# Optimization experiments

Hardware: AMD Instinct MI355X
Metric: run time of the kernel (lower is better)

Reference implementation:

```python
import jax, jax.numpy as jnp
import numpy as np

N_CELLS = 1024
HID = 256
IN_DIM = 256
OUT_DIM = 256
NOISE_DIM = 32
N_LOOP = 32  # min(32, n_cells)


def _lin(x, W, b):
    # torch nn.Linear: y = x @ W.T + b, W shape [out, in]
    return x @ W.T + b


def faction_sync_debate(h, step, n_factions=8, sync=0.15, debate=0.15):
    n, d = h.shape
    n_f = min(n_factions, n // 2)
    if n_f < 2:
        return h
    fs = n // n_f  # assumes n_f * fs == n (true for 1024/8)
    blk = h.reshape(n_f, fs, d)
    # per-faction mean pull (disjoint slices -> order independent)
    blk = (1.0 - sync) * blk + sync * blk.mean(axis=1, keepdims=True)
    if step > 5:  # step is a Python int -> static branch
        global_opinion = blk.mean(axis=1).mean(axis=0)  # [d]
        dc = max(1, fs // 4)
        blk = blk.at[:, :dc, :].set((1.0 - debate) * blk[:, :dc, :] + debate * global_opinion)
    return blk.reshape(n, d)


def setup_inputs() -> dict:
    key = jax.random.key(0)
    ks = iter(jax.random.split(key, 32))

    def rn(shape, scale=0.02):
        return (jax.random.normal(next(ks), shape, dtype=jnp.float32) * scale)

    flat = N_CELLS * HID  # 262144
    inp = {
        "x": rn((1, IN_DIM), 1.0),
        "noise": rn((1, NOISE_DIM), 1.0),
        "cell_hiddens": rn((N_CELLS, HID), 0.1),
        # generator: Linear(in+32,256) -> ReLU -> Linear(256,512) -> ReLU -> Linear(512, flat)
        "gen_W1": rn((256, IN_DIM + NOISE_DIM)), "gen_b1": rn((256,)),
        "gen_W2": rn((512, 256)), "gen_b2": rn((512,)),
        "gen_W3": rn((flat, 512)), "gen_b3": rn((flat,)),
        # discriminator: Linear(flat,512) -> LReLU(0.2) -> Linear(512,256) -> LReLU -> Linear(256,1) -> Sigmoid
        "disc_W1": rn((512, flat)), "disc_b1": rn((512,)),
        "disc_W2": rn((256, 512)), "disc_b2": rn((256,)),
        "disc_W3": rn((1, 256)), "disc_b3": rn((1,)),
        # mind engines: Linear(in+hid,128) -> ReLU -> Linear(128,out)
        "ea_W1": rn((128, IN_DIM + HID)), "ea_b1": rn((128,)),
        "ea_W2": rn((OUT_DIM, 128)), "ea_b2": rn((OUT_DIM,)),
        "eg_W1": rn((128, IN_DIM + HID)), "eg_b1": rn((128,)),
        "eg_W2": rn((OUT_DIM, 128)), "eg_b2": rn((OUT_DIM,)),
        # GRUCell(out+1, hid): gate order r, z, n
        "gru_Wih": rn((3 * HID, OUT_DIM + 1)), "gru_bih": rn((3 * HID,)),
        "gru_Whh": rn((3 * HID, HID)), "gru_bhh": rn((3 * HID,)),
        "step": 10,
    }
    return inp


def reference(x, noise, cell_hiddens,
              gen_W1, gen_b1, gen_W2, gen_b2, gen_W3, gen_b3,
              disc_W1, disc_b1, disc_W2, disc_b2, disc_W3, disc_b3,
              ea_W1, ea_b1, ea_W2, ea_b2, eg_W1, eg_b1, eg_W2, eg_b2,
              gru_Wih, gru_bih, gru_Whh, gru_bhh, step):
    sg = jax.lax.stop_gradient
    # --- generate_states ---
    gi = jnp.concatenate([x, noise], axis=-1)           # [1, in+32]
    h1 = jax.nn.relu(_lin(gi, gen_W1, gen_b1))
    h2 = jax.nn.relu(_lin(h1, gen_W2, gen_b2))
    gen_states = _lin(h2, gen_W3, gen_b3).reshape(N_CELLS, HID)
    # torch: gen_states.detach() then faction sync+debate
    synced = faction_sync_debate(sg(gen_states), step)
    # --- batched BenchMind over first 32 cells (replaces Python loop) ---
    H = synced[:N_LOOP]                                  # [32, HID]
    X = jnp.broadcast_to(x, (N_LOOP, x.shape[-1]))       # [32, IN]
    comb = jnp.concatenate([X, H], axis=-1)              # [32, IN+HID]
    a = _lin(jax.nn.relu(_lin(comb, ea_W1, ea_b1)), ea_W2, ea_b2)
    g = _lin(jax.nn.relu(_lin(comb, eg_W1, eg_b1)), eg_W2, eg_b2)
    outputs = a - g                                      # [32, OUT]
    tensions = (outputs ** 2).mean(axis=-1)              # [32]
    # GRUCell update (mem inputs detached as in torch)
    mem_in = jnp.concatenate([sg(outputs), sg(tensions)[:, None]], axis=-1)  # [32, OUT+1]
    gih = _lin(mem_in, gru_Wih, gru_bih)
    ghh = _lin(H, gru_Whh, gru_bhh)
    ir, iz, i_n = jnp.split(gih, 3, axis=-1)
    hr, hz, h_n = jnp.split(ghh, 3, axis=-1)
    r = jax.nn.sigmoid(ir + hr)
    z = jax.nn.sigmoid(iz + hz)
    n_cand = jnp.tanh(i_n + r * h_n)
    new_hiddens = (1.0 - z) * n_cand + z * H             # [32, HID]
    # --- buffer update (no_grad) + discriminate ---
    new_cell_hiddens = sg(0.7 * synced + 0.3 * cell_hiddens)

    def disc(s):
        f = s.reshape(1, -1)
        d1 = jax.nn.leaky_relu(_lin(f, disc_W1, disc_b1), 0.2)
        d2 = jax.nn.leaky_relu(_lin(d1, disc_W2, disc_b2), 0.2)
        return jax.nn.sigmoid(_lin(d2, disc_W3, disc_b3))

    d_real = disc(new_cell_hiddens)
    d_fake = disc(gen_states)
    # tensions were .item()'d in torch -> constants
    mean_tension = sg(tensions).mean()
    w = jax.nn.softmax(sg(tensions))                     # [32]
    combined = (w[:, None] * outputs).sum(axis=0, keepdims=True)  # [1, OUT]
    return combined, mean_tension, d_real, d_fake, new_hiddens
```

## Files before the change

### kernel.cpp

```cpp
#include <hip/hip_runtime.h>
#include <math.h>

#define N_CELLS 1024
#define HID     256
#define IN_DIM  256
#define NOISE_DIM 32
#define OUT_DIM 256
#define N_LOOP  32
#define FLAT    (N_CELLS*HID)

__device__ __forceinline__ float wave_reduce64(float v) {
    #pragma unroll
    for (int m = 32; m; m >>= 1) v += __shfl_xor(v, m);
    return v;
}

__global__ void k_gen_h1(const float* __restrict__ x, const float* __restrict__ noise,
                         const float* __restrict__ W1, const float* __restrict__ b1,
                         float* __restrict__ h1) {
    __shared__ __align__(16) float gi[288];
    int t = threadIdx.x, l = t & 63, w = t >> 6;
    gi[t] = x[t];
    if (t < 32) gi[256 + t] = noise[t];
    __syncthreads();
    int j = blockIdx.x * 4 + w;
    const float4* wr = (const float4*)(W1 + j * 288);
    const float4* g4 = (const float4*)gi;
    float4 a = wr[l], v = g4[l];
    float acc = a.x*v.x + a.y*v.y + a.z*v.z + a.w*v.w;
    if (l < 8) {
        float4 a2 = wr[64 + l], v2 = g4[64 + l];
        acc += a2.x*v2.x + a2.y*v2.y + a2.z*v2.z + a2.w*v2.w;
    }
    acc = wave_reduce64(acc);
    if (l == 0) h1[j] = fmaxf(acc + b1[j], 0.f);
}

__global__ void k_gen_h2(const float* __restrict__ h1, const float* __restrict__ W2,
                         const float* __restrict__ b2, float* __restrict__ h2) {
    int t = threadIdx.x, l = t & 63, w = t >> 6;
    int j = blockIdx.x * 4 + w;
    float4 a = ((const float4*)(W2 + j * 256))[l];
    float4 v = ((const float4*)h1)[l];
    float acc = a.x*v.x + a.y*v.y + a.z*v.z + a.w*v.w;
    acc = wave_reduce64(acc);
    if (l == 0) h2[j] = fmaxf(acc + b2[j], 0.f);
}

__global__ void k_gen_big(const float* __restrict__ W3, const float* __restrict__ b3,
                          const float* __restrict__ h2, float* __restrict__ gs) {
    int lane = threadIdx.x & 63;
    int row  = blockIdx.x * (blockDim.x >> 6) + (threadIdx.x >> 6);
    const float4* h24 = (const float4*)h2;
    float4 ha = h24[lane], hb = h24[64 + lane];
    const float4* w4 = (const float4*)(W3 + (size_t)row * 512);
    float4 wa = w4[lane], wb = w4[64 + lane];
    float acc = wa.x*ha.x + wa.y*ha.y + wa.z*ha.z + wa.w*ha.w
              + wb.x*hb.x + wb.y*hb.y + wb.z*hb.z + wb.w*hb.w;
    acc = wave_reduce64(acc);
    if (lane == 0) gs[row] = acc + b3[row];
}

__global__ void k_fmean(const float* __restrict__ gs, float* __restrict__ fmean) {
    __shared__ float part[4][64];
    int b = blockIdx.x, t = threadIdx.x;
    int f = b >> 2, q = b & 3;
    int c = q * 64 + (t & 63), rg = t >> 6;
    const float* base = gs + (size_t)(f * 128 + rg * 32) * 256 + c;
    float s = 0.f;
    for (int i = 0; i < 32; ++i) s += base[(size_t)i * 256];
    part[rg][t & 63] = s;
    __syncthreads();
    if (t < 64) {
        float v = part[0][t] + part[1][t] + part[2][t] + part[3][t];
        fmean[f * 256 + q * 64 + t] = v * (1.f / 128.f);
    }
}

__global__ void k_sync(const float* __restrict__ gs, const float* __restrict__ fmean,
                       const float* __restrict__ ch, const int* __restrict__ step,
                       float* __restrict__ Hbuf, float* __restrict__ ncn) {
    int c = blockIdx.x, d = threadIdx.x;
    int f = c >> 7;
    float gm = 0.f;
    #pragma unroll
    for (int k = 0; k < 8; ++k) gm += fmean[k * 256 + d];
    gm *= 0.125f;
    float fm = fmean[f * 256 + d];
    float v = 0.85f * gs[c * 256 + d] + 0.15f * fm;
    if (((c & 127) < 32) && (*step > 5)) v = 0.85f * v + 0.15f * gm;
    ncn[c * 256 + d] = 0.7f * v + 0.3f * ch[c * 256 + d];
    if (c < N_LOOP) Hbuf[c * 256 + d] = v;
}

__global__ void k_mega(const float* __restrict__ dW1, const float* __restrict__ db1,
                       const float* __restrict__ ncn, const float* __restrict__ gs,
                       const float* __restrict__ x, const float* __restrict__ Hbuf,
                       const float* __restrict__ eaW1, const float* __restrict__ eab1,
                       const float* __restrict__ eaW2, const float* __restrict__ eab2,
                       const float* __restrict__ egW1, const float* __restrict__ egb1,
                       const float* __restrict__ egW2, const float* __restrict__ egb2,
                       const float* __restrict__ Wih, const float* __restrict__ bih,
                       const float* __restrict__ Whh, const float* __restrict__ bhh,
                       float* __restrict__ d1r, float* __restrict__ d1f,
                       float* __restrict__ outputs, float* __restrict__ tensions,
                       float* __restrict__ out) {
    __shared__ float sR[16];
    __shared__ float sF[16];
    __shared__ __align__(16) float xh[512];
    __shared__ __align__(16) float hag[256];
    __shared__ __align__(16) float outs[256];
    __shared__ float red[256];
    __shared__ float rzA[512];
    __shared__ float inb[256];
    __shared__ float hnb[256];
    __shared__ float tsh;
    int b = blockIdx.x, t = threadIdx.x, l = t & 63, w = t >> 6;

    if (b >= 32) {
        int row = b - 32;
        const float4* w4 = (const float4*)(dW1 + (size_t)row * FLAT);
        const float4* r4 = (const float4*)ncn;
        const float4* f4 = (const float4*)gs;
        float aR = 0.f, aF = 0.f;
        for (int i = t; i < FLAT / 4; i += 1024) {
            float4 ww = w4[i], r = r4[i], f = f4[i];
            aR += ww.x*r.x + ww.y*r.y + ww.z*r.z + ww.w*r.w;
            aF += ww.x*f.x + ww.y*f.y + ww.z*f.z + ww.w*f.w;
        }
        aR = wave_reduce64(aR);
        aF = wave_reduce64(aF);
        if (l == 0) { sR[w] = aR; sF[w] = aF; }
        __syncthreads();
        if (t < 16) {
            float r = sR[t], f = sF[t];
            #pragma unroll
            for (int m = 8; m; m >>= 1) { r += __shfl_xor(r, m); f += __shfl_xor(f, m); }
            if (t == 0) { d1r[row] = r + db1[row]; d1f[row] = f + db1[row]; }
        }
        return;
    }

    int i = b;
    if (t < 512) xh[t] = (t < 256) ? x[t] : Hbuf[i * 256 + (t - 256)];
    __syncthreads();

    for (int k = 0; k < 16; ++k) {
        int j = w * 16 + k;
        const float* W = (j < 128) ? (eaW1 + (size_t)j * 512) : (egW1 + (size_t)(j - 128) * 512);
        const float4* w4 = (const float4*)W;
        const float4* v4 = (const float4*)xh;
        float4 a = w4[l], v = v4[l];
        float acc = a.x*v.x + a.y*v.y + a.z*v.z + a.w*v.w;
        float4 a2 = w4[64 + l], v2 = v4[64 + l];
        acc += a2.x*v2.x + a2.y*v2.y + a2.z*v2.z + a2.w*v2.w;
        acc = wave_reduce64(acc);
        if (l == 0) {
            float bias = (j < 128) ? eab1[j] : egb1[j - 128];
            hag[j] = fmaxf(acc + bias, 0.f);
        }
    }
    __syncthreads();

    for (int k = 0; k < 16; ++k) {
        int tr = w * 16 + k;
        int sl = l & 31;
        bool lo = (l < 32);
        const float4* wv4 = lo ? (const float4*)(eaW2 + (size_t)tr * 128)
                               : (const float4*)(egW2 + (size_t)tr * 128);
        const float4* h4 = (const float4*)(hag + (lo ? 0 : 128));
        float4 a = wv4[sl], v = h4[sl];
        float d_ = a.x*v.x + a.y*v.y + a.z*v.z + a.w*v.w;
        float acc = lo ? d_ : -d_;
        acc = wave_reduce64(acc);
        if (l == 0) {
            float o = acc + eab2[tr] - egb2[tr];
            outs[tr] = o;
            outputs[i * 256 + tr] = o;
        }
    }
    __syncthreads();

    if (t < 256) red[t] = outs[t] * outs[t];
    __syncthreads();
    for (int m = 128; m; m >>= 1) { if (t < m && t + m < 256) red[t] += red[t + m]; __syncthreads(); }
    if (t == 0) { float tn = red[0] * (1.f / 256.f); tensions[i] = tn; tsh = tn; }
    __syncthreads();
    float tn = tsh;

    {
        float4 ov = ((const float4*)outs)[l];
        float4 Hv = ((const float4*)(xh + 256))[l];
        for (int k = 0; k < 48; ++k) {
            int u = w * 48 + k;
            const float* wr = Wih + (size_t)u * 257;
            float g0 = wr[4*l]*ov.x + wr[4*l+1]*ov.y + wr[4*l+2]*ov.z + wr[4*l+3]*ov.w;
            if (l == 0) g0 += wr[256] * tn;
            float4 wh = ((const float4*)(Whh + (size_t)u * 256))[l];
            float h0 = wh.x*Hv.x + wh.y*Hv.y + wh.z*Hv.z + wh.w*Hv.w;
            if (u < 512) {
                float s = wave_reduce64(g0 + h0);
                if (l == 0) rzA[u] = s + bih[u] + bhh[u];
            } else {
                float sg = wave_reduce64(g0);
                float sh = wave_reduce64(h0);
                if (l == 0) { inb[u - 512] = sg + bih[u]; hnb[u - 512] = sh + bhh[u]; }
            }
        }
    }
    __syncthreads();

    if (t < 256) {
        float r = 1.f / (1.f + expf(-rzA[t]));
        float z = 1.f / (1.f + expf(-rzA[256 + t]));
        float nc = tanhf(inb[t] + r * hnb[t]);
        float Hd = xh[256 + t];
        out[259 + i * 256 + t] = (1.f - z) * nc + z * Hd;
    }
}

__global__ void k_epi(const float* __restrict__ W2, const float* __restrict__ b2,
                      const float* __restrict__ W3, const float* __restrict__ b3,
                      const float* __restrict__ d1r, const float* __restrict__ d1f,
                      const float* __restrict__ outputs, const float* __restrict__ tensions,
                      float* __restrict__ out) {
    int b = blockIdx.x, t = threadIdx.x;
    if (b < 2) {
        __shared__ __align__(16) float lv[512];
        __shared__ float l2[256];
        __shared__ float red[256];
        const float* d1 = b ? d1f : d1r;
        for (int j = t; j < 512; j += 256) { float v = d1[j]; lv[j] = v > 0.f ? v : 0.2f * v; }
        __syncthreads();
        {
            float acc = b2[t];
            const float4* wr = (const float4*)(W2 + t * 512);
            const float4* l4 = (const float4*)lv;
            for (int k = 0; k < 128; ++k) {
                float4 w = wr[k], v = l4[k];
                acc += w.x*v.x + w.y*v.y + w.z*v.z + w.w*v.w;
            }
            l2[t] = acc > 0.f ? acc : 0.2f * acc;
        }
        __syncthreads();
        red[t] = l2[t] * W3[t];
        __syncthreads();
        for (int m = 128; m; m >>= 1) { if (t < m) red[t] += red[t + m]; __syncthreads(); }
        if (t == 0) { float v = red[0] + b3[0]; out[257 + b] = 1.f / (1.f + expf(-v)); }
    } else {
        __shared__ float w[32];
        __shared__ float ts[32];
        if (t < 32) ts[t] = tensions[t];
        __syncthreads();
        if (t == 0) {
            float mx = ts[0];
            for (int i = 1; i < 32; ++i) mx = fmaxf(mx, ts[i]);
            float s = 0.f, mean = 0.f;
            for (int i = 0; i < 32; ++i) { float e = expf(ts[i] - mx); w[i] = e; s += e; mean += ts[i]; }
            float inv = 1.f / s;
            for (int i = 0; i < 32; ++i) w[i] *= inv;
            out[256] = mean * (1.f / 32.f);
        }
        __syncthreads();
        float c = 0.f;
        for (int i = 0; i < 32; ++i) c += w[i] * outputs[i * 256 + t];
        out[t] = c;
    }
}

extern "C" void kernel_launch(void* const* d_in, const int* in_sizes, int n_in,
                              void* d_out, int out_size, void* d_ws, size_t ws_size,
                              hipStream_t stream) {
    const float* x     = (const float*)d_in[0];
    const float* noise = (const float*)d_in[1];
    const float* ch    = (const float*)d_in[2];
    const float* gW1   = (const float*)d_in[3];
    const float* gb1   = (const float*)d_in[4];
    const float* gW2   = (const float*)d_in[5];
    const float* gb2   = (const float*)d_in[6];
    const float* gW3   = (const float*)d_in[7];
    const float* gb3   = (const float*)d_in[8];
    const float* dW1   = (const float*)d_in[9];
    const float* db1   = (const float*)d_in[10];
    const float* dW2   = (const float*)d_in[11];
    const float* db2   = (const float*)d_in[12];
    const float* dW3   = (const float*)d_in[13];
    const float* db3   = (const float*)d_in[14];
    const float* eaW1  = (const float*)d_in[15];
    const float* eab1  = (const float*)d_in[16];
    const float* eaW2  = (const float*)d_in[17];
    const float* eab2  = (const float*)d_in[18];
    const float* egW1  = (const float*)d_in[19];
    const float* egb1  = (const float*)d_in[20];
    const float* egW2  = (const float*)d_in[21];
    const float* egb2  = (const float*)d_in[22];
    const float* Wih   = (const float*)d_in[23];
    const float* bih   = (const float*)d_in[24];
    const float* Whh   = (const float*)d_in[25];
    const float* bhh   = (const float*)d_in[26];
    const int*   step  = (const int*)d_in[27];

    float* out = (float*)d_out;
    float* ws  = (float*)d_ws;
    float* h1buf    = ws;
    float* h2       = h1buf + 256;
    float* gs       = h2 + 512;
    float* ncn      = gs + 262144;
    float* fmean    = ncn + 262144;
    float* Hbuf     = fmean + 2048;
    float* outputs  = Hbuf + 8192;
    float* tensions = outputs + 8192;
    float* d1r      = tensions + 32;
    float* d1f      = d1r + 512;

    k_gen_h1<<<64, 256, 0, stream>>>(x, noise, gW1, gb1, h1buf);
    k_gen_h2<<<128, 256, 0, stream>>>(h1buf, gW2, gb2, h2);
    k_gen_big<<<FLAT / 4, 256, 0, stream>>>(gW3, gb3, h2, gs);
    k_fmean<<<32, 256, 0, stream>>>(gs, fmean);
    k_sync<<<1024, 256, 0, stream>>>(gs, fmean, ch, step, Hbuf, ncn);
    k_mega<<<544, 1024, 0, stream>>>(dW1, db1, ncn, gs, x, Hbuf,
                                     eaW1, eab1, eaW2, eab2,
                                     egW1, egb1, egW2, egb2,
                                     Wih, bih, Whh, bhh,
                                     d1r, d1f, outputs, tensions, out);
    k_epi<<<3, 256, 0, stream>>>(dW2, db2, dW3, db3, d1r, d1f, outputs, tensions, out);
}
```

Measured before the change: 292.6 us.

## Fuse faction sync into discriminator kernel, batch gen rows, split epilogue

The separate sync kernel that wrote the 1 MB ncn and Hbuf buffers is removed. The discriminator blocks now recompute the synced and new cell hiddens on the fly from gs, ch and the faction means held in shared memory, and the engine blocks rebuild their H row directly. The big generator GEMV now computes four rows per wave and writes them with a vectorized store. The fmean loop is unrolled into four accumulators, and the epilogue is split into an 8-block layer-2 GEMV plus a 1-block tail. This saves one launch and a large write/read round trip, at the cost of extra ALU work and one more epilogue launch.

Result: no change. 295.8 us (+1.1%).

```diff
diff --git a/kernel.cpp b/kernel.cpp
--- a/kernel.cpp
+++ b/kernel.cpp
@@ -14,6 +14,9 @@
     for (int m = 32; m; m >>= 1) v += __shfl_xor(v, m);
     return v;
 }
+__device__ __forceinline__ float dot4(float4 a, float4 b) {
+    return a.x*b.x + a.y*b.y + a.z*b.z + a.w*b.w;
+}
 
 __global__ void k_gen_h1(const float* __restrict__ x, const float* __restrict__ noise,
                          const float* __restrict__ W1, const float* __restrict__ b1,
@@ -27,10 +30,10 @@
     const float4* wr = (const float4*)(W1 + j * 288);
     const float4* g4 = (const float4*)gi;
     float4 a = wr[l], v = g4[l];
-    float acc = a.x*v.x + a.y*v.y + a.z*v.z + a.w*v.w;
+    float acc = dot4(a, v);
     if (l < 8) {
         float4 a2 = wr[64 + l], v2 = g4[64 + l];
-        acc += a2.x*v2.x + a2.y*v2.y + a2.z*v2.z + a2.w*v2.w;
+        acc += dot4(a2, v2);
     }
     acc = wave_reduce64(acc);
     if (l == 0) h1[j] = fmaxf(acc + b1[j], 0.f);
@@ -42,23 +45,41 @@
     int j = blockIdx.x * 4 + w;
     float4 a = ((const float4*)(W2 + j * 256))[l];
     float4 v = ((const float4*)h1)[l];
-    float acc = a.x*v.x + a.y*v.y + a.z*v.z + a.w*v.w;
+    float acc = dot4(a, v);
     acc = wave_reduce64(acc);
     if (l == 0) h2[j] = fmaxf(acc + b2[j], 0.f);
 }
 
 __global__ void k_gen_big(const float* __restrict__ W3, const float* __restrict__ b3,
                           const float* __restrict__ h2, float* __restrict__ gs) {
-    int lane = threadIdx.x & 63;
-    int row  = blockIdx.x * (blockDim.x >> 6) + (threadIdx.x >> 6);
+    int t = threadIdx.x, l = t & 63, w = t >> 6;
+    int r0 = blockIdx.x * 16 + w * 4;
     const float4* h24 = (const float4*)h2;
-    float4 ha = h24[lane], hb = h24[64 + lane];
-    const float4* w4 = (const float4*)(W3 + (size_t)row * 512);
-    float4 wa = w4[lane], wb = w4[64 + lane];
-    float acc = wa.x*ha.x + wa.y*ha.y + wa.z*ha.z + wa.w*ha.w
-              + wb.x*hb.x + wb.y*hb.y + wb.z*hb.z + wb.w*hb.w;
-    acc = wave_reduce64(acc);
-    if (lane == 0) gs[row] = acc + b3[row];
+    float4 ha = h24[l], hb = h24[64 + l];
+    float4 A0, A1, A2, A3, B0, B1, B2, B3;
+    {
+        const float4* w0 = (const float4*)(W3 + (size_t)(r0 + 0) * 512);
+        const float4* w1 = (const float4*)(W3 + (size_t)(r0 + 1) * 512);
+        const float4* w2 = (const float4*)(W3 + (size_t)(r0 + 2) * 512);
+        const float4* w3 = (const float4*)(W3 + (size_t)(r0 + 3) * 512);
+        A0 = w0[l]; B0 = w0[64 + l];
+        A1 = w1[l]; B1 = w1[64 + l];
+        A2 = w2[l]; B2 = w2[64 + l];
+        A3 = w3[l]; B3 = w3[64 + l];
+    }
+    float s0 = dot4(A0, ha) + dot4(B0, hb);
+    float s1 = dot4(A1, ha) + dot4(B1, hb);
+    float s2 = dot4(A2, ha) + dot4(B2, hb);
+    float s3 = dot4(A3, ha) + dot4(B3, hb);
+    s0 = wave_reduce64(s0);
+    s1 = wave_reduce64(s1);
+    s2 = wave_reduce64(s2);
+    s3 = wave_reduce64(s3);
+    if (l == 0) {
+        float4 bv = *(const float4*)(b3 + r0);
+        float4 o; o.x = s0 + bv.x; o.y = s1 + bv.y; o.z = s2 + bv.z; o.w = s3 + bv.w;
+        *(float4*)(gs + r0) = o;
+    }
 }
 
 __global__ void k_fmean(const float* __restrict__ gs, float* __restrict__ fmean) {
@@ -67,9 +88,14 @@
     int f = b >> 2, q = b & 3;
     int c = q * 64 + (t & 63), rg = t >> 6;
     const float* base = gs + (size_t)(f * 128 + rg * 32) * 256 + c;
-    float s = 0.f;
-    for (int i = 0; i < 32; ++i) s += base[(size_t)i * 256];
-    part[rg][t & 63] = s;
+    float s0 = 0.f, s1 = 0.f, s2 = 0.f, s3 = 0.f;
+    for (int i = 0; i < 32; i += 4) {
+        s0 += base[(size_t)(i + 0) * 256];
+        s1 += base[(size_t)(i + 1) * 256];
+        s2 += base[(size_t)(i + 2) * 256];
+        s3 += base[(size_t)(i + 3) * 256];
+    }
+    part[rg][t & 63] = (s0 + s1) + (s2 + s3);
     __syncthreads();
     if (t < 64) {
         float v = part[0][t] + part[1][t] + part[2][t] + part[3][t];
@@ -77,25 +103,10 @@
     }
 }
 
-__global__ void k_sync(const float* __restrict__ gs, const float* __restrict__ fmean,
-                       const float* __restrict__ ch, const int* __restrict__ step,
-                       float* __restrict__ Hbuf, float* __restrict__ ncn) {
-    int c = blockIdx.x, d = threadIdx.x;
-    int f = c >> 7;
-    float gm = 0.f;
-    #pragma unroll
-    for (int k = 0; k < 8; ++k) gm += fmean[k * 256 + d];
-    gm *= 0.125f;
-    float fm = fmean[f * 256 + d];
-    float v = 0.85f * gs[c * 256 + d] + 0.15f * fm;
-    if (((c & 127) < 32) && (*step > 5)) v = 0.85f * v + 0.15f * gm;
-    ncn[c * 256 + d] = 0.7f * v + 0.3f * ch[c * 256 + d];
-    if (c < N_LOOP) Hbuf[c * 256 + d] = v;
-}
-
 __global__ void k_mega(const float* __restrict__ dW1, const float* __restrict__ db1,
-                       const float* __restrict__ ncn, const float* __restrict__ gs,
-                       const float* __restrict__ x, const float* __restrict__ Hbuf,
+                       const float* __restrict__ gs, const float* __restrict__ ch,
+                       const float* __restrict__ fmean, const int* __restrict__ step,
+                       const float* __restrict__ x,
                        const float* __restrict__ eaW1, const float* __restrict__ eab1,
                        const float* __restrict__ eaW2, const float* __restrict__ eab2,
                        const float* __restrict__ egW1, const float* __restrict__ egb1,
@@ -107,6 +118,8 @@
                        float* __restrict__ out) {
     __shared__ float sR[16];
     __shared__ float sF[16];
+    __shared__ __align__(16) float fmL[2048];
+    __shared__ __align__(16) float gmL[256];
     __shared__ __align__(16) float xh[512];
     __shared__ __align__(16) float hag[256];
     __shared__ __align__(16) float outs[256];
@@ -116,17 +129,46 @@
     __shared__ float hnb[256];
     __shared__ float tsh;
     int b = blockIdx.x, t = threadIdx.x, l = t & 63, w = t >> 6;
+    bool deb = (*step > 5);
 
     if (b >= 32) {
+        for (int i = t; i < 2048; i += 1024) fmL[i] = fmean[i];
+        __syncthreads();
+        if (t < 256) {
+            float g = 0.f;
+            #pragma unroll
+            for (int f = 0; f < 8; ++f) g += fmL[f * 256 + t];
+            gmL[t] = g * 0.125f;
+        }
+        __syncthreads();
         int row = b - 32;
         const float4* w4 = (const float4*)(dW1 + (size_t)row * FLAT);
-        const float4* r4 = (const float4*)ncn;
-        const float4* f4 = (const float4*)gs;
+        const float4* g4 = (const float4*)gs;
+        const float4* c4 = (const float4*)ch;
         float aR = 0.f, aF = 0.f;
         for (int i = t; i < FLAT / 4; i += 1024) {
-            float4 ww = w4[i], r = r4[i], f = f4[i];
-            aR += ww.x*r.x + ww.y*r.y + ww.z*r.z + ww.w*r.w;
-            aF += ww.x*f.x + ww.y*f.y + ww.z*f.z + ww.w*f.w;
+            int c = i >> 6, d4 = i & 63;
+            float4 ww = w4[i], gv = g4[i], cv = c4[i];
+            float4 fmv = *(const float4*)(fmL + ((c >> 7) << 8) + d4 * 4);
+            float4 v;
+            v.x = 0.85f * gv.x + 0.15f * fmv.x;
+            v.y = 0.85f * gv.y + 0.15f * fmv.y;
+            v.z = 0.85f * gv.z + 0.15f * fmv.z;
+            v.w = 0.85f * gv.w + 0.15f * fmv.w;
+            if (deb && ((c & 127) < 32)) {
+                float4 gm = *(const float4*)(gmL + d4 * 4);
+                v.x = 0.85f * v.x + 0.15f * gm.x;
+                v.y = 0.85f * v.y + 0.15f * gm.y;
+                v.z = 0.85f * v.z + 0.15f * gm.z;
+                v.w = 0.85f * v.w + 0.15f * gm.w;
+            }
+            float4 nc;
+            nc.x = 0.7f * v.x + 0.3f * cv.x;
+            nc.y = 0.7f * v.y + 0.3f * cv.y;
+            nc.z = 0.7f * v.z + 0.3f * cv.z;
+            nc.w = 0.7f * v.w + 0.3f * cv.w;
+            aR += dot4(ww, nc);
+            aF += dot4(ww, gv);
         }
         aR = wave_reduce64(aR);
         aF = wave_reduce64(aF);
@@ -142,7 +184,17 @@
     }
 
     int i = b;
-    if (t < 512) xh[t] = (t < 256) ? x[t] : Hbuf[i * 256 + (t - 256)];
+    if (t < 256) {
+        xh[t] = x[t];
+        float g = gs[i * 256 + t];
+        float gmv = 0.f;
+        #pragma unroll
+        for (int f = 0; f < 8; ++f) gmv += fmean[f * 256 + t];
+        gmv *= 0.125f;
+        float v = 0.85f * g + 0.15f * fmean[t];
+        if (deb) v = 0.85f * v + 0.15f * gmv;
+        xh[256 + t] = v;
+    }
     __syncthreads();
 
     for (int k = 0; k < 16; ++k) {
@@ -150,10 +202,7 @@
         const float* W = (j < 128) ? (eaW1 + (size_t)j * 512) : (egW1 + (size_t)(j - 128) * 512);
         const float4* w4 = (const float4*)W;
         const float4* v4 = (const float4*)xh;
-        float4 a = w4[l], v = v4[l];
-        float acc = a.x*v.x + a.y*v.y + a.z*v.z + a.w*v.w;
-        float4 a2 = w4[64 + l], v2 = v4[64 + l];
-        acc += a2.x*v2.x + a2.y*v2.y + a2.z*v2.z + a2.w*v2.w;
+        float acc = dot4(w4[l], v4[l]) + dot4(w4[64 + l], v4[64 + l]);
         acc = wave_reduce64(acc);
         if (l == 0) {
             float bias = (j < 128) ? eab1[j] : egb1[j - 128];
@@ -169,8 +218,7 @@
         const float4* wv4 = lo ? (const float4*)(eaW2 + (size_t)tr * 128)
                                : (const float4*)(egW2 + (size_t)tr * 128);
         const float4* h4 = (const float4*)(hag + (lo ? 0 : 128));
-        float4 a = wv4[sl], v = h4[sl];
-        float d_ = a.x*v.x + a.y*v.y + a.z*v.z + a.w*v.w;
+        float d_ = dot4(wv4[sl], h4[sl]);
         float acc = lo ? d_ : -d_;
         acc = wave_reduce64(acc);
         if (l == 0) {
@@ -197,7 +245,7 @@
             float g0 = wr[4*l]*ov.x + wr[4*l+1]*ov.y + wr[4*l+2]*ov.z + wr[4*l+3]*ov.w;
             if (l == 0) g0 += wr[256] * tn;
             float4 wh = ((const float4*)(Whh + (size_t)u * 256))[l];
-            float h0 = wh.x*Hv.x + wh.y*Hv.y + wh.z*Hv.z + wh.w*Hv.w;
+            float h0 = dot4(wh, Hv);
             if (u < 512) {
                 float s = wave_reduce64(g0 + h0);
                 if (l == 0) rzA[u] = s + bih[u] + bhh[u];
@@ -219,53 +267,59 @@
     }
 }
 
-__global__ void k_epi(const float* __restrict__ W2, const float* __restrict__ b2,
-                      const float* __restrict__ W3, const float* __restrict__ b3,
-                      const float* __restrict__ d1r, const float* __restrict__ d1f,
-                      const float* __restrict__ outputs, const float* __restrict__ tensions,
-                      float* __restrict__ out) {
-    int b = blockIdx.x, t = threadIdx.x;
-    if (b < 2) {
-        __shared__ __align__(16) float lv[512];
-        __shared__ float l2[256];
-        __shared__ float red[256];
-        const float* d1 = b ? d1f : d1r;
-        for (int j = t; j < 512; j += 256) { float v = d1[j]; lv[j] = v > 0.f ? v : 0.2f * v; }
-        __syncthreads();
-        {
-            float acc = b2[t];
-            const float4* wr = (const float4*)(W2 + t * 512);
-            const float4* l4 = (const float4*)lv;
-            for (int k = 0; k < 128; ++k) {
-                float4 w = wr[k], v = l4[k];
-                acc += w.x*v.x + w.y*v.y + w.z*v.z + w.w*v.w;
-            }
-            l2[t] = acc > 0.f ? acc : 0.2f * acc;
-        }
-        __syncthreads();
-        red[t] = l2[t] * W3[t];
+__global__ void k_epi1(const float* __restrict__ W2, const float* __restrict__ b2,
+                       const float* __restrict__ d1r, const float* __restrict__ d1f,
+                       float* __restrict__ l2buf) {
+    __shared__ __align__(16) float lv[512];
+    int b = blockIdx.x, t = threadIdx.x, l = t & 63, w = t >> 6;
+    int br = b >> 2, q = b & 3;
+    const float* d1 = br ? d1f : d1r;
+    for (int j = t; j < 512; j += 256) { float v = d1[j]; lv[j] = v > 0.f ? v : 0.2f * v; }
+    __syncthreads();
+    const float4* l4 = (const float4*)lv;
+    float4 va = l4[l], vb = l4[64 + l];
+    for (int k = 0; k < 16; ++k) {
+        int tr = q * 64 + w * 16 + k;
+        const float4* wr = (const float4*)(W2 + (size_t)tr * 512);
+        float acc = dot4(wr[l], va) + dot4(wr[64 + l], vb);
+        acc = wave_reduce64(acc);
+        if (l == 0) {
+            float z = acc + b2[tr];
+            l2buf[br * 256 + tr] = z > 0.f ? z : 0.2f * z;
+        }
+    }
+}
+
+__global__ void k_epi2(const float* __restrict__ W3, const float* __restrict__ b3,
+                       const float* __restrict__ l2buf,
+                       const float* __restrict__ outputs, const float* __restrict__ tensions,
+                       float* __restrict__ out) {
+    __shared__ float red[256];
+    __shared__ float w[32];
+    __shared__ float ts[32];
+    int t = threadIdx.x;
+    for (int p = 0; p < 2; ++p) {
+        red[t] = l2buf[p * 256 + t] * W3[t];
         __syncthreads();
         for (int m = 128; m; m >>= 1) { if (t < m) red[t] += red[t + m]; __syncthreads(); }
-        if (t == 0) { float v = red[0] + b3[0]; out[257 + b] = 1.f / (1.f + expf(-v)); }
-    } else {
-        __shared__ float w[32];
-        __shared__ float ts[32];
-        if (t < 32) ts[t] = tensions[t];
-        __syncthreads();
-        if (t == 0) {
-            float mx = ts[0];
-            for (int i = 1; i < 32; ++i) mx = fmaxf(mx, ts[i]);
-            float s = 0.f, mean = 0.f;
-            for (int i = 0; i < 32; ++i) { float e = expf(ts[i] - mx); w[i] = e; s += e; mean += ts[i]; }
-            float inv = 1.f / s;
-            for (int i = 0; i < 32; ++i) w[i] *= inv;
-            out[256] = mean * (1.f / 32.f);
-        }
-        __syncthreads();
-        float c = 0.f;
-        for (int i = 0; i < 32; ++i) c += w[i] * outputs[i * 256 + t];
-        out[t] = c;
-    }
+        if (t == 0) out[257 + p] = 1.f / (1.f + expf(-(red[0] + b3[0])));
+        __syncthreads();
+    }
+    if (t < 32) ts[t] = tensions[t];
+    __syncthreads();
+    if (t == 0) {
+        float mx = ts[0];
+        for (int i = 1; i < 32; ++i) mx = fmaxf(mx, ts[i]);
+        float s = 0.f, mean = 0.f;
+        for (int i = 0; i < 32; ++i) { float e = expf(ts[i] - mx); w[i] = e; s += e; mean += ts[i]; }
+        float inv = 1.f / s;
+        for (int i = 0; i < 32; ++i) w[i] *= inv;
+        out[256] = mean * (1.f / 32.f);
+    }
+    __syncthreads();
+    float c = 0.f;
+    for (int i = 0; i < 32; ++i) c += w[i] * outputs[i * 256 + t];
+    out[t] = c;
 }
 
 extern "C" void kernel_launch(void* const* d_in, const int* in_sizes, int n_in,
@@ -305,23 +359,22 @@
     float* h1buf    = ws;
     float* h2       = h1buf + 256;
     float* gs       = h2 + 512;
-    float* ncn      = gs + 262144;
-    float* fmean    = ncn + 262144;
-    float* Hbuf     = fmean + 2048;
-    float* outputs  = Hbuf + 8192;
+    float* fmean    = gs + 262144;
+    float* outputs  = fmean + 2048;
     float* tensions = outputs + 8192;
     float* d1r      = tensions + 32;
     float* d1f      = d1r + 512;
+    float* l2buf    = d1f + 512;
 
     k_gen_h1<<<64, 256, 0, stream>>>(x, noise, gW1, gb1, h1buf);
     k_gen_h2<<<128, 256, 0, stream>>>(h1buf, gW2, gb2, h2);
-    k_gen_big<<<FLAT / 4, 256, 0, stream>>>(gW3, gb3, h2, gs);
+    k_gen_big<<<FLAT / 16, 256, 0, stream>>>(gW3, gb3, h2, gs);
     k_fmean<<<32, 256, 0, stream>>>(gs, fmean);
-    k_sync<<<1024, 256, 0, stream>>>(gs, fmean, ch, step, Hbuf, ncn);
-    k_mega<<<544, 1024, 0, stream>>>(dW1, db1, ncn, gs, x, Hbuf,
+    k_mega<<<544, 1024, 0, stream>>>(dW1, db1, gs, ch, fmean, step, x,
                                      eaW1, eab1, eaW2, eab2,
                                      egW1, egb1, egW2, egb2,
                                      Wih, bih, Whh, bhh,
                                      d1r, d1f, outputs, tensions, out);
-    k_epi<<<3, 256, 0, stream>>>(dW2, db2, dW3, db3, d1r, d1f, outputs, tensions, out);
-}
+    k_epi1<<<8, 256, 0, stream>>>(dW2, db2, d1r, d1f, l2buf);
+    k_epi2<<<1, 256, 0, stream>>>(dW3, db3, l2buf, outputs, tensions, out);
+}
```
